# Optimization experiments

Measured on AMD Instinct MI355X. Metric: run time of the kernel, lower is better.

The kernel has to match this reference:

```python
import jax, jax.numpy as jnp
import numpy as np

# QuantumConv2d from ESPCN-PyTorch (quantum variant).
# QuantumLinear(kH, kW, ...) is a parameterized quantum circuit mapping a flattened
# kH*kW patch to kH Z-expectation values. We model the standard single-qubit-per-row
# RY-chain circuit: out[k] = cos( sum_w patch[k, w] + theta[k] )  (Z expectation after
# sequential RY rotations by the kW row inputs plus one trainable angle per row).
# The conv then averages the kH outputs and sums over input channels, exactly as the
# torch forward does. We replicate the original's circuits[i*j] indexing (i=out ch,
# j=in ch), and use cos(a+b)=cos a cos b - sin a sin b to turn the channel/row
# reduction into two dense einsums (same math, efficient expression).

KH, KW = 3, 3
PH, PW = 1, 1
OC = 32


def setup_inputs() -> dict:
    key = jax.random.key(0)
    k1, k2 = jax.random.split(key)
    x = jax.random.normal(k1, (8, 16, 128, 128), dtype=jnp.float32)
    # one circuit per (out_ch, in_ch, kernel_row): oC*iC*kH = 32*16*3 = 1536, kH params each
    theta = jax.random.normal(k2, (OC * 16 * KH, KH), dtype=jnp.float32)
    return {"x": x, "theta": theta}


def _row_window_sums(x):
    # x: (n, iC, H, W) -> (n, iC, kH, oH, oW): sum over the kW window for each kernel row
    xp = jnp.pad(x, ((0, 0), (0, 0), (PH, PH), (PW, PW)))
    Hp, Wp = xp.shape[2], xp.shape[3]
    oH, oW = Hp - (KH - 1), Wp - (KW - 1)
    rows = []
    for k in range(KH):  # tiny fixed loop over kernel rows
        s = xp[:, :, k:k + oH, 0:oW]
        for w in range(1, KW):
            s = s + xp[:, :, k:k + oH, w:w + oW]
        rows.append(s)
    return jnp.stack(rows, axis=2)


def reference(x, theta):
    n, iC = x.shape[0], x.shape[1]
    R = _row_window_sums(x)  # (n, iC, kH, oH, oW) angle sums per patch row
    # replicate torch's self.circuits[i * j] lookup
    idx = jnp.arange(OC)[:, None] * jnp.arange(iC)[None, :]  # (oC, iC)
    th = theta[idx]  # (oC, iC, kH)
    # out[n,i,h,w] = sum_j mean_k cos(R[n,j,k,h,w] + th[i,j,k])
    out = (jnp.einsum('njkhw,ijk->nihw', jnp.cos(R), jnp.cos(th))
           - jnp.einsum('njkhw,ijk->nihw', jnp.sin(R), jnp.sin(th))) / KH
    return out
```

## Files before the change

### kernel.cpp

```cpp
#include <hip/hip_runtime.h>

#define OC 32
#define IC 16
#define HH 128
#define WW 128
#define NB 8
#define STRIDE_DW 52

typedef __attribute__((ext_vector_type(8))) __bf16 bf16x8;
typedef __attribute__((ext_vector_type(4))) float f32x4;

#define INV_2PI 0.15915494309189535f

__device__ inline unsigned int pack2bf(float lo, float hi) {
    union { __bf16 h[2]; unsigned int u; } p;
    p.h[0] = (__bf16)lo;
    p.h[1] = (__bf16)hi;
    return p.u;
}

__device__ inline void hw_sincos(float rad, float* sn, float* cs) {
    float rev = rad * INV_2PI;
    float fr = rev - floorf(rev);
    *sn = __builtin_amdgcn_sinf(fr);
    *cs = __builtin_amdgcn_cosf(fr);
}

__global__ __launch_bounds__(256, 4) void qconv_kernel(
        const float* __restrict__ x,
        const float* __restrict__ theta,
        float* __restrict__ out) {
    __shared__ unsigned int A_lds[OC * STRIDE_DW];
    __shared__ unsigned int B_lds[128 * STRIDE_DW];

    const int tx = threadIdx.x;
    const int ty = threadIdx.y;
    const int t  = ty * 64 + tx;

    const int bid = blockIdx.x;
    const int wbase = (bid & 1) * 64;
    const int hp = (bid >> 1) & 63;
    const int n  = bid >> 7;
    const int h0 = hp * 2;
    const int w  = wbase + tx;

    const float inv3 = 1.0f / 3.0f;
#pragma unroll
    for (int q = t; q < OC * 48; q += 256) {
        int m  = q >> 5;
        int oc = q & 31;
        int j  = m / 3;
        int kk = m - 3 * j;
        float th = theta[(oc * j) * 3 + kk];
        float sn, cs;
        hw_sincos(th, &sn, &cs);
        A_lds[oc * STRIDE_DW + m] = pack2bf(cs * inv3, -sn * inv3);
    }

    const float* xn = x + (size_t)n * IC * HH * WW;
    const int r = h0 - 1 + ty;
    const bool valid = (r >= 0) && (r < HH);
    const bool wlok = (w > 0), wrok = (w < WW - 1);

#pragma unroll
    for (int j = 0; j < IC; ++j) {
        float s = 0.f;
        if (valid) {
            const float* row = xn + ((size_t)j * HH + r) * WW;
            float c0 = row[w];
            float cm = wlok ? row[w - 1] : 0.f;
            float cp = wrok ? row[w + 1] : 0.f;
            s = cm + c0 + cp;
        }
        float sn, cs;
        hw_sincos(s, &sn, &cs);
        unsigned int pk = pack2bf(cs, sn);
        if (ty < 3)  B_lds[(tx)      * STRIDE_DW + 3 * j + ty]     = pk;
        if (ty >= 1) B_lds[(64 + tx) * STRIDE_DW + 3 * j + ty - 1] = pk;
    }
    __syncthreads();

    const int l15 = tx & 15;
    const int lk  = tx >> 4;
    const char* Ab = (const char*)A_lds;
    const char* Bb = (const char*)B_lds;

    f32x4 acc[2][2];
#pragma unroll
    for (int a = 0; a < 2; ++a)
#pragma unroll
        for (int b = 0; b < 2; ++b) acc[a][b] = (f32x4){0.f, 0.f, 0.f, 0.f};

#pragma unroll
    for (int Kt = 0; Kt < 3; ++Kt) {
        bf16x8 afr[2], bfr[2];
#pragma unroll
        for (int Mt = 0; Mt < 2; ++Mt)
            afr[Mt] = *(const bf16x8*)(Ab + (l15 + 16 * Mt) * 208 + Kt * 64 + lk * 16);
#pragma unroll
        for (int Nt = 0; Nt < 2; ++Nt)
            bfr[Nt] = *(const bf16x8*)(Bb + (ty * 32 + 16 * Nt + l15) * 208 + Kt * 64 + lk * 16);
#pragma unroll
        for (int Mt = 0; Mt < 2; ++Mt)
#pragma unroll
            for (int Nt = 0; Nt < 2; ++Nt)
                acc[Mt][Nt] = __builtin_amdgcn_mfma_f32_16x16x32_bf16(
                    afr[Mt], bfr[Nt], acc[Mt][Nt], 0, 0, 0);
    }

#pragma unroll
    for (int Mt = 0; Mt < 2; ++Mt)
#pragma unroll
        for (int Nt = 0; Nt < 2; ++Nt)
#pragma unroll
            for (int e = 0; e < 4; ++e) {
                int oc = 16 * Mt + lk * 4 + e;
                int px = ty * 32 + 16 * Nt + l15;
                int hrow = px >> 6, wloc = px & 63;
                out[(((size_t)n * OC + oc) * HH + (h0 + hrow)) * WW + (wbase + wloc)]
                    = acc[Mt][Nt][e];
            }
}

extern "C" void kernel_launch(void* const* d_in, const int* in_sizes, int n_in,
                              void* d_out, int out_size, void* d_ws, size_t ws_size,
                              hipStream_t stream) {
    const float* x     = (const float*)d_in[0];
    const float* theta = (const float*)d_in[1];
    float* out = (float*)d_out;

    dim3 block(64, 4, 1);
    int nblocks = NB * (HH / 2) * 2;
    qconv_kernel<<<nblocks, block, 0, stream>>>(x, theta, out);
}
```

Measured before the change: 73.65 us.

## Split trig precompute into separate kernel writing packed sincos to workspace

Moves the row-window sum and sin/cos evaluation into a first kernel that writes packed bf16 (cos, sin) planes with padded rows, plus the theta-derived A matrix, to global workspace. The GEMM kernel then gathers MFMA fragments directly from global memory without LDS or a barrier. This avoids recomputing the theta trig per block and avoids recomputing halo rows twice, but adds a second launch and a round trip of a ~4 MB intermediate through memory, with scattered 4-byte gathers.

New measurement: 74.37 us. About the same (+1.0%).

```diff
diff --git a/kernel.cpp b/kernel.cpp
--- a/kernel.cpp
+++ b/kernel.cpp
@@ -5,7 +5,12 @@
 #define HH 128
 #define WW 128
 #define NB 8
-#define STRIDE_DW 52
+#define RP 130
+#define PLANE (RP * WW)
+#define TRIG_DW (NB * IC * PLANE)
+#define A_OFF TRIG_DW
+#define A_DW (OC * 48)
+#define TOTAL_DW (TRIG_DW + A_DW)
 
 typedef __attribute__((ext_vector_type(8))) __bf16 bf16x8;
 typedef __attribute__((ext_vector_type(4))) float f32x4;
@@ -26,64 +31,97 @@
     *cs = __builtin_amdgcn_cosf(fr);
 }
 
-__global__ __launch_bounds__(256, 4) void qconv_kernel(
-        const float* __restrict__ x,
-        const float* __restrict__ theta,
+__global__ void trig_kernel(const float* __restrict__ x,
+                            const float* __restrict__ theta,
+                            unsigned int* __restrict__ ws) {
+    int idx = blockIdx.x * 256 + threadIdx.x;
+    if (idx >= TOTAL_DW) return;
+
+    if (idx < TRIG_DW) {
+        int w = idx & (WW - 1);
+        int rowidx = idx >> 7;
+        int rp = rowidx % RP;
+        int pj = rowidx / RP;
+        unsigned int pk;
+        int r = rp - 1;
+        if (r >= 0 && r < HH) {
+            const float* row = x + ((size_t)pj * HH + r) * WW;
+            float c0 = row[w];
+            float cm = (w > 0)      ? row[w - 1] : 0.f;
+            float cp = (w < WW - 1) ? row[w + 1] : 0.f;
+            float s = cm + c0 + cp;
+            float sn, cs;
+            hw_sincos(s, &sn, &cs);
+            pk = pack2bf(cs, sn);
+        } else {
+            pk = 0x00003F80u;
+        }
+        ws[idx] = pk;
+    } else {
+        int q = idx - A_OFF;
+        int oc = q / 48;
+        int m = q - oc * 48;
+        int j = m / 3;
+        int kk = m - 3 * j;
+        float th = theta[(oc * j) * 3 + kk];
+        float sn, cs;
+        hw_sincos(th, &sn, &cs);
+        const float inv3 = 1.0f / 3.0f;
+        ws[idx] = pack2bf(cs * inv3, -sn * inv3);
+    }
+}
+
+__global__ __launch_bounds__(256, 4) void gemm_kernel(
+        const unsigned int* __restrict__ ws,
         float* __restrict__ out) {
-    __shared__ unsigned int A_lds[OC * STRIDE_DW];
-    __shared__ unsigned int B_lds[128 * STRIDE_DW];
-
     const int tx = threadIdx.x;
     const int ty = threadIdx.y;
-    const int t  = ty * 64 + tx;
 
     const int bid = blockIdx.x;
     const int wbase = (bid & 1) * 64;
     const int hp = (bid >> 1) & 63;
     const int n  = bid >> 7;
     const int h0 = hp * 2;
-    const int w  = wbase + tx;
-
-    const float inv3 = 1.0f / 3.0f;
-#pragma unroll
-    for (int q = t; q < OC * 48; q += 256) {
-        int m  = q >> 5;
-        int oc = q & 31;
-        int j  = m / 3;
-        int kk = m - 3 * j;
-        float th = theta[(oc * j) * 3 + kk];
-        float sn, cs;
-        hw_sincos(th, &sn, &cs);
-        A_lds[oc * STRIDE_DW + m] = pack2bf(cs * inv3, -sn * inv3);
-    }
-
-    const float* xn = x + (size_t)n * IC * HH * WW;
-    const int r = h0 - 1 + ty;
-    const bool valid = (r >= 0) && (r < HH);
-    const bool wlok = (w > 0), wrok = (w < WW - 1);
-
-#pragma unroll
-    for (int j = 0; j < IC; ++j) {
-        float s = 0.f;
-        if (valid) {
-            const float* row = xn + ((size_t)j * HH + r) * WW;
-            float c0 = row[w];
-            float cm = wlok ? row[w - 1] : 0.f;
-            float cp = wrok ? row[w + 1] : 0.f;
-            s = cm + c0 + cp;
-        }
-        float sn, cs;
-        hw_sincos(s, &sn, &cs);
-        unsigned int pk = pack2bf(cs, sn);
-        if (ty < 3)  B_lds[(tx)      * STRIDE_DW + 3 * j + ty]     = pk;
-        if (ty >= 1) B_lds[(64 + tx) * STRIDE_DW + 3 * j + ty - 1] = pk;
-    }
-    __syncthreads();
 
     const int l15 = tx & 15;
     const int lk  = tx >> 4;
-    const char* Ab = (const char*)A_lds;
-    const char* Bb = (const char*)B_lds;
+
+    const unsigned int* At = ws + A_OFF;
+
+    union U4 { unsigned int u[4]; bf16x8 h; };
+    bf16x8 afr[3][2];
+#pragma unroll
+    for (int Kt = 0; Kt < 3; ++Kt)
+#pragma unroll
+        for (int Mt = 0; Mt < 2; ++Mt) {
+            U4 a;
+            const unsigned int* p = At + (l15 + 16 * Mt) * 48 + Kt * 16 + lk * 4;
+#pragma unroll
+            for (int e = 0; e < 4; ++e) a.u[e] = p[e];
+            afr[Kt][Mt] = a.h;
+        }
+
+    bf16x8 bfr[3][2];
+#pragma unroll
+    for (int Nt = 0; Nt < 2; ++Nt) {
+        int px = ty * 32 + 16 * Nt + l15;
+        int hrow = px >> 6;
+        int w = wbase + (px & 63);
+        const unsigned int* base = ws + (size_t)n * IC * PLANE + w;
+#pragma unroll
+        for (int Kt = 0; Kt < 3; ++Kt) {
+            U4 b;
+#pragma unroll
+            for (int e = 0; e < 4; ++e) {
+                int m = Kt * 16 + lk * 4 + e;
+                int j = m / 3;
+                int kk = m - 3 * j;
+                int rp = h0 + hrow + kk;
+                b.u[e] = base[(size_t)j * PLANE + rp * WW];
+            }
+            bfr[Kt][Nt] = b.h;
+        }
+    }
 
     f32x4 acc[2][2];
 #pragma unroll
@@ -92,21 +130,13 @@
         for (int b = 0; b < 2; ++b) acc[a][b] = (f32x4){0.f, 0.f, 0.f, 0.f};
 
 #pragma unroll
-    for (int Kt = 0; Kt < 3; ++Kt) {
-        bf16x8 afr[2], bfr[2];
-#pragma unroll
-        for (int Mt = 0; Mt < 2; ++Mt)
-            afr[Mt] = *(const bf16x8*)(Ab + (l15 + 16 * Mt) * 208 + Kt * 64 + lk * 16);
-#pragma unroll
-        for (int Nt = 0; Nt < 2; ++Nt)
-            bfr[Nt] = *(const bf16x8*)(Bb + (ty * 32 + 16 * Nt + l15) * 208 + Kt * 64 + lk * 16);
+    for (int Kt = 0; Kt < 3; ++Kt)
 #pragma unroll
         for (int Mt = 0; Mt < 2; ++Mt)
 #pragma unroll
             for (int Nt = 0; Nt < 2; ++Nt)
                 acc[Mt][Nt] = __builtin_amdgcn_mfma_f32_16x16x32_bf16(
-                    afr[Mt], bfr[Nt], acc[Mt][Nt], 0, 0, 0);
-    }
+                    afr[Kt][Mt], bfr[Kt][Nt], acc[Mt][Nt], 0, 0, 0);
 
 #pragma unroll
     for (int Mt = 0; Mt < 2; ++Mt)
@@ -128,8 +158,10 @@
     const float* x     = (const float*)d_in[0];
     const float* theta = (const float*)d_in[1];
     float* out = (float*)d_out;
+    unsigned int* ws = (unsigned int*)d_ws;
+
+    trig_kernel<<<(TOTAL_DW + 255) / 256, 256, 0, stream>>>(x, theta, ws);
 
     dim3 block(64, 4, 1);
-    int nblocks = NB * (HH / 2) * 2;
-    qconv_kernel<<<nblocks, block, 0, stream>>>(x, theta, out);
+    gemm_kernel<<<NB * (HH / 2) * 2, block, 0, stream>>>(ws, out);
 }
```
